# Optimization experiments

Hardware: AMD Instinct MI355X
Metric: run time of the kernel (lower is better)

The kernel has to match this reference:

```python
import jax, jax.numpy as jnp
import numpy as np

B, S, D = 8, 1024, 768
H, HD = 12, 64  # heads, head dim (H*HD == D)
EPS = 1e-12


def setup_inputs() -> dict:
    key = jax.random.key(0)
    ks = jax.random.split(key, 8)
    s = 0.02
    return {
        "hidden_states": jax.random.normal(ks[0], (B, S, D), jnp.float32),
        "attention_mask": jnp.zeros((B, 1, 1, S), jnp.float32),
        "head_mask": jnp.ones((H,), jnp.float32),
        "Wq": jax.random.normal(ks[1], (D, H * HD), jnp.float32) * s,
        "bq": jnp.zeros((H * HD,), jnp.float32),
        "Wk": jax.random.normal(ks[2], (D, H * HD), jnp.float32) * s,
        "bk": jnp.zeros((H * HD,), jnp.float32),
        "Wv": jax.random.normal(ks[3], (D, H * HD), jnp.float32) * s,
        "bv": jnp.zeros((H * HD,), jnp.float32),
        "Wo": jax.random.normal(ks[4], (D, H * HD), jnp.float32) * s,  # torch Linear weight [out=D, in=H*HD]
        "bo": jnp.zeros((D,), jnp.float32),
        "gamma": jnp.ones((D,), jnp.float32),
        "beta": jnp.zeros((D,), jnp.float32),
    }


def reference(hidden_states, attention_mask, head_mask, Wq, bq, Wk, bk, Wv, bv, Wo, bo, gamma, beta):
    def heads(x):  # [B,S,H*HD] -> [B,H,S,HD]
        return x.reshape(B, S, H, HD).transpose(0, 2, 1, 3)

    q = heads(hidden_states @ Wq.T + bq)
    k = heads(hidden_states @ Wk.T + bk)
    v = heads(hidden_states @ Wv.T + bv)

    scores = jnp.einsum("bhqd,bhkd->bhqk", q, k) / np.sqrt(HD).astype(np.float32)
    scores = scores + attention_mask
    probs = jax.nn.softmax(scores, axis=-1)  # dropout p=0 (eval)
    ctx = jnp.einsum("bhqk,bhkd->bhqd", probs, v)  # [B,H,S,HD]

    # masked per-head output projection: Wo.T.view(H, HD, D)
    Wph = Wo.T.reshape(H, HD, D)
    proj = jnp.einsum("bhsd,hde,h->bse", ctx, Wph, head_mask) + bo

    # residual + LayerNorm
    x = proj + hidden_states
    mu = jnp.mean(x, axis=-1, keepdims=True)
    var = jnp.mean(jnp.square(x - mu), axis=-1, keepdims=True)
    out = (x - mu) * jax.lax.rsqrt(var + EPS) * gamma + beta
    return out
```

## Files before the change

### kernel.cpp

```cpp
#include <hip/hip_runtime.h>
#include <hip/hip_bf16.h>
#include <math.h>

#define Bn 8
#define Sn 1024
#define Dn 768
#define Hn 12
#define MROWS (Bn * Sn)

typedef __attribute__((ext_vector_type(8))) short short8;
typedef __attribute__((ext_vector_type(4))) float floatx4;

__device__ __forceinline__ unsigned short f2b(float x) {
    union { float f; unsigned u; } v; v.f = x;
    unsigned r = v.u + 0x7fffu + ((v.u >> 16) & 1u);
    return (unsigned short)(r >> 16);
}

__device__ __forceinline__ void gload16(const void* g, void* l) {
    __builtin_amdgcn_global_load_lds(
        (const __attribute__((address_space(1))) void*)g,
        (__attribute__((address_space(3))) void*)l, 16, 0, 0);
}

__global__ __launch_bounds__(256) void convert_all(const float* __restrict__ X,
                                                   const float* __restrict__ Wq, const float* __restrict__ Wk,
                                                   const float* __restrict__ Wv, const float* __restrict__ Wo,
                                                   unsigned short* __restrict__ Xb,
                                                   unsigned short* __restrict__ Wqb, unsigned short* __restrict__ Wkb,
                                                   unsigned short* __restrict__ Wvb, unsigned short* __restrict__ Wob) {
    const int id = blockIdx.x;
    const float* src;
    unsigned short* dst;
    int i;
    if (id < 6144) {
        src = X; dst = Xb;
        i = id * 256 + threadIdx.x;
    } else {
        const int y = (id - 6144) / 576;
        src = (y == 0) ? Wq : (y == 1) ? Wk : (y == 2) ? Wv : Wo;
        dst = (y == 0) ? Wqb : (y == 1) ? Wkb : (y == 2) ? Wvb : Wob;
        i = ((id - 6144) % 576) * 256 + threadIdx.x;
    }
    float4 v = reinterpret_cast<const float4*>(src)[i];
    ushort4 o;
    o.x = f2b(v.x); o.y = f2b(v.y); o.z = f2b(v.z); o.w = f2b(v.w);
    reinterpret_cast<ushort4*>(dst)[i] = o;
}

__global__ __launch_bounds__(256) void gemm_qkv(const unsigned short* __restrict__ A,
                                                const unsigned short* __restrict__ Wq,
                                                const unsigned short* __restrict__ Wk,
                                                const unsigned short* __restrict__ Wv,
                                                const float* __restrict__ bq,
                                                const float* __restrict__ bk,
                                                const float* __restrict__ bv,
                                                unsigned short* __restrict__ Qh,
                                                unsigned short* __restrict__ Kh,
                                                unsigned short* __restrict__ Vt) {
    __shared__ __align__(16) unsigned short As[128 * 64];
    __shared__ __align__(16) unsigned short Ws[128 * 64];
    const int id = blockIdx.x;
    const int by = id & 63;
    const int bx = id >> 6;
    const int mat = bx / 6;
    const int m0 = by * 128;
    const int n0 = (bx % 6) * 128;
    const unsigned short* W = (mat == 0) ? Wq : (mat == 1) ? Wk : Wv;
    const float* bias = (mat == 0) ? bq : (mat == 1) ? bk : bv;
    unsigned short* Cout = (mat == 0) ? Qh : (mat == 1) ? Kh : Vt;

    const int tid = threadIdx.x;
    const int w = tid >> 6, l = tid & 63, quad = l >> 4, mr = l & 15;
    const int wm = (w >> 1) * 64, wn = (w & 1) * 64;

    const unsigned short* gAsrc[4];
    const unsigned short* gWsrc[4];
    unsigned short* lAdst[4];
    unsigned short* lWdst[4];
#pragma unroll
    for (int j = 0; j < 4; j++) {
        const int u = tid + j * 256;
        const int r = u >> 3, c = u & 7;
        const int kq = (c ^ (r & 7)) * 8;
        gAsrc[j] = &A[(size_t)(m0 + r) * Dn + kq];
        gWsrc[j] = &W[(size_t)(n0 + r) * Dn + kq];
        lAdst[j] = &As[u * 8];
        lWdst[j] = &Ws[u * 8];
    }

    int aoff[4][2], woff[4][2];
#pragma unroll
    for (int i = 0; i < 4; i++) {
        const int ra = wm + i * 16 + mr;
        const int rw = wn + i * 16 + mr;
#pragma unroll
        for (int ks = 0; ks < 2; ks++) {
            aoff[i][ks] = (ra * 8 + ((quad + ks * 4) ^ (ra & 7))) * 8;
            woff[i][ks] = (rw * 8 + ((quad + ks * 4) ^ (rw & 7))) * 8;
        }
    }

    floatx4 acc[4][4];
#pragma unroll
    for (int i = 0; i < 4; i++)
#pragma unroll
        for (int j = 0; j < 4; j++) {
            floatx4 z = {0.f, 0.f, 0.f, 0.f};
            acc[i][j] = z;
        }

    for (int kt = 0; kt < 12; kt++) {
        const int k0 = kt * 64;
        __syncthreads();
#pragma unroll
        for (int j = 0; j < 4; j++) {
            gload16(gAsrc[j] + k0, lAdst[j]);
            gload16(gWsrc[j] + k0, lWdst[j]);
        }
        __syncthreads();

        short8 af[4][2], bf[4][2];
#pragma unroll
        for (int i = 0; i < 4; i++)
#pragma unroll
            for (int ks = 0; ks < 2; ks++) {
                af[i][ks] = *(const short8*)&As[aoff[i][ks]];
                bf[i][ks] = *(const short8*)&Ws[woff[i][ks]];
            }
#pragma unroll
        for (int ks = 0; ks < 2; ks++)
#pragma unroll
            for (int i = 0; i < 4; i++)
#pragma unroll
                for (int j = 0; j < 4; j++)
                    acc[i][j] = __builtin_amdgcn_mfma_f32_16x16x32_bf16(af[i][ks], bf[j][ks], acc[i][j], 0, 0, 0);
    }

#pragma unroll
    for (int j = 0; j < 4; j++) {
        const int col = n0 + wn + j * 16 + mr;
        const float bval = bias[col];
        const int h = col >> 6, d = col & 63;
#pragma unroll
        for (int i = 0; i < 4; i++) {
#pragma unroll
            for (int r = 0; r < 4; r++) {
                const int m = m0 + wm + i * 16 + quad * 4 + r;
                const float val = acc[i][j][r] + bval;
                const int b = m >> 10, s = m & 1023;
                const size_t base = (size_t)(b * Hn + h) << 16;
                if (mat == 2)
                    Cout[base + (size_t)d * 1024 + s] = f2b(val);
                else
                    Cout[base + (size_t)s * 64 + d] = f2b(val);
            }
        }
    }
}

__global__ __launch_bounds__(256) void gemm_out(const unsigned short* __restrict__ A,
                                                const unsigned short* __restrict__ W,
                                                const float* __restrict__ bias,
                                                const float* __restrict__ X,
                                                float* __restrict__ xres) {
    __shared__ __align__(16) unsigned short As[64 * 64];
    __shared__ __align__(16) unsigned short Ws[128 * 64];
    const int id = blockIdx.x;
    const int by = id & 127;
    const int bx = id >> 7;
    const int m0 = by * 64;
    const int n0 = bx * 128;

    const int tid = threadIdx.x;
    const int w = tid >> 6, l = tid & 63, quad = l >> 4, mr = l & 15;

    const unsigned short* gAsrc[2];
    unsigned short* lAdst[2];
#pragma unroll
    for (int j = 0; j < 2; j++) {
        const int u = tid + j * 256;
        const int r = u >> 3, c = u & 7;
        gAsrc[j] = &A[(size_t)(m0 + r) * Dn + (c ^ (r & 7)) * 8];
        lAdst[j] = &As[u * 8];
    }
    const unsigned short* gWsrc[4];
    unsigned short* lWdst[4];
#pragma unroll
    for (int j = 0; j < 4; j++) {
        const int u = tid + j * 256;
        const int r = u >> 3, c = u & 7;
        gWsrc[j] = &W[(size_t)(n0 + r) * Dn + (c ^ (r & 7)) * 8];
        lWdst[j] = &Ws[u * 8];
    }

    int aoff[4][2], woff[2][2];
#pragma unroll
    for (int i = 0; i < 4; i++) {
        const int ra = i * 16 + mr;
#pragma unroll
        for (int ks = 0; ks < 2; ks++)
            aoff[i][ks] = (ra * 8 + ((quad + ks * 4) ^ (ra & 7))) * 8;
    }
#pragma unroll
    for (int j = 0; j < 2; j++) {
        const int rw = w * 32 + j * 16 + mr;
#pragma unroll
        for (int ks = 0; ks < 2; ks++)
            woff[j][ks] = (rw * 8 + ((quad + ks * 4) ^ (rw & 7))) * 8;
    }

    floatx4 acc[4][2];
#pragma unroll
    for (int i = 0; i < 4; i++)
#pragma unroll
        for (int j = 0; j < 2; j++) {
            floatx4 z = {0.f, 0.f, 0.f, 0.f};
            acc[i][j] = z;
        }

    for (int kt = 0; kt < 12; kt++) {
        const int k0 = kt * 64;
        __syncthreads();
#pragma unroll
        for (int j = 0; j < 2; j++) gload16(gAsrc[j] + k0, lAdst[j]);
#pragma unroll
        for (int j = 0; j < 4; j++) gload16(gWsrc[j] + k0, lWdst[j]);
        __syncthreads();

        short8 af[4][2], bf[2][2];
#pragma unroll
        for (int i = 0; i < 4; i++)
#pragma unroll
            for (int ks = 0; ks < 2; ks++)
                af[i][ks] = *(const short8*)&As[aoff[i][ks]];
#pragma unroll
        for (int j = 0; j < 2; j++)
#pragma unroll
            for (int ks = 0; ks < 2; ks++)
                bf[j][ks] = *(const short8*)&Ws[woff[j][ks]];
#pragma unroll
        for (int ks = 0; ks < 2; ks++)
#pragma unroll
            for (int i = 0; i < 4; i++)
#pragma unroll
                for (int j = 0; j < 2; j++)
                    acc[i][j] = __builtin_amdgcn_mfma_f32_16x16x32_bf16(af[i][ks], bf[j][ks], acc[i][j], 0, 0, 0);
    }

#pragma unroll
    for (int j = 0; j < 2; j++) {
        const int col = n0 + w * 32 + j * 16 + mr;
        const float bval = bias[col];
#pragma unroll
        for (int i = 0; i < 4; i++) {
#pragma unroll
            for (int r = 0; r < 4; r++) {
                const int m = m0 + i * 16 + quad * 4 + r;
                xres[(size_t)m * Dn + col] = acc[i][j][r] + bval + X[(size_t)m * Dn + col];
            }
        }
    }
}

__global__ __launch_bounds__(256) void flash_attn_mfma(const unsigned short* __restrict__ Qh,
                                                       const unsigned short* __restrict__ Kh,
                                                       const unsigned short* __restrict__ Vt,
                                                       const float* __restrict__ mask,
                                                       const float* __restrict__ head_mask,
                                                       unsigned short* __restrict__ ctx) {
    __shared__ __align__(16) unsigned short Ks[64 * 72];
    __shared__ __align__(16) unsigned short Vs[64 * 72];
    __shared__ __align__(16) unsigned short Ps[128 * 72];
    __shared__ float msk[64];

    const int id = blockIdx.x;
    const int bh = id % 96;
    const int qt = id / 96;
    const int b = bh / Hn, h = bh % Hn;
    const int q0 = qt * 128;
    const int tid = threadIdx.x;
    const int w = tid >> 6, l = tid & 63, quad = l >> 4, mr = l & 15;
    const size_t hb = (size_t)(b * Hn + h) << 16;

    short8 aq[2][2];
#pragma unroll
    for (int i = 0; i < 2; i++)
#pragma unroll
        for (int ks = 0; ks < 2; ks++)
            aq[i][ks] = *(const short8*)&Qh[hb + (size_t)(q0 + w * 32 + i * 16 + mr) * 64 + ks * 32 + quad * 8];

    float l_s[2][4];
    floatx4 oacc[2][4];
#pragma unroll
    for (int i = 0; i < 2; i++) {
#pragma unroll
        for (int r = 0; r < 4; r++) l_s[i][r] = 0.f;
#pragma unroll
        for (int jj = 0; jj < 4; jj++) {
            floatx4 z = {0.f, 0.f, 0.f, 0.f};
            oacc[i][jj] = z;
        }
    }

    const int srow = tid >> 2;
    const int scol = (tid & 3) * 16;

    short8 pk0 = *(const short8*)&Kh[hb + (size_t)srow * 64 + scol];
    short8 pk1 = *(const short8*)&Kh[hb + (size_t)srow * 64 + scol + 8];
    short8 pv0 = *(const short8*)&Vt[hb + (size_t)srow * 1024 + scol];
    short8 pv1 = *(const short8*)&Vt[hb + (size_t)srow * 1024 + scol + 8];
    float pm = mask[b * Sn + (tid & 63)];

    for (int kt = 0; kt < Sn / 64; kt++) {
        __syncthreads();
        *(short8*)&Ks[srow * 72 + scol] = pk0;
        *(short8*)&Ks[srow * 72 + scol + 8] = pk1;
        *(short8*)&Vs[srow * 72 + scol] = pv0;
        *(short8*)&Vs[srow * 72 + scol + 8] = pv1;
        if (tid < 64) msk[tid] = pm;
        if (kt < Sn / 64 - 1) {
            const int k0 = (kt + 1) * 64;
            pk0 = *(const short8*)&Kh[hb + (size_t)(k0 + srow) * 64 + scol];
            pk1 = *(const short8*)&Kh[hb + (size_t)(k0 + srow) * 64 + scol + 8];
            pv0 = *(const short8*)&Vt[hb + (size_t)srow * 1024 + k0 + scol];
            pv1 = *(const short8*)&Vt[hb + (size_t)srow * 1024 + k0 + scol + 8];
            pm = mask[b * Sn + k0 + (tid & 63)];
        }
        __syncthreads();

        floatx4 sacc[2][4];
#pragma unroll
        for (int i = 0; i < 2; i++)
#pragma unroll
            for (int j = 0; j < 4; j++) {
                floatx4 z = {0.f, 0.f, 0.f, 0.f};
                sacc[i][j] = z;
            }
#pragma unroll
        for (int ks = 0; ks < 2; ks++) {
#pragma unroll
            for (int j = 0; j < 4; j++) {
                short8 bk = *(const short8*)&Ks[(j * 16 + mr) * 72 + ks * 32 + quad * 8];
                sacc[0][j] = __builtin_amdgcn_mfma_f32_16x16x32_bf16(aq[0][ks], bk, sacc[0][j], 0, 0, 0);
                sacc[1][j] = __builtin_amdgcn_mfma_f32_16x16x32_bf16(aq[1][ks], bk, sacc[1][j], 0, 0, 0);
            }
        }

#pragma unroll
        for (int i = 0; i < 2; i++) {
#pragma unroll
            for (int j = 0; j < 4; j++) {
                const float mk = msk[j * 16 + mr];
#pragma unroll
                for (int r = 0; r < 4; r++) {
                    const float p = __expf(sacc[i][j][r] * 0.125f + mk);
                    l_s[i][r] += p;
                    Ps[(w * 32 + i * 16 + quad * 4 + r) * 72 + j * 16 + mr] = f2b(p);
                }
            }
        }

#pragma unroll
        for (int ks = 0; ks < 2; ks++) {
            short8 ap0 = *(const short8*)&Ps[(w * 32 + mr) * 72 + ks * 32 + quad * 8];
            short8 ap1 = *(const short8*)&Ps[(w * 32 + 16 + mr) * 72 + ks * 32 + quad * 8];
#pragma unroll
            for (int jj = 0; jj < 4; jj++) {
                short8 bv = *(const short8*)&Vs[(jj * 16 + mr) * 72 + ks * 32 + quad * 8];
                oacc[0][jj] = __builtin_amdgcn_mfma_f32_16x16x32_bf16(ap0, bv, oacc[0][jj], 0, 0, 0);
                oacc[1][jj] = __builtin_amdgcn_mfma_f32_16x16x32_bf16(ap1, bv, oacc[1][jj], 0, 0, 0);
            }
        }
    }

    const float hm = head_mask[h];
    float inv[2][4];
#pragma unroll
    for (int i = 0; i < 2; i++)
#pragma unroll
        for (int r = 0; r < 4; r++) {
            float t = l_s[i][r];
            t += __shfl_xor(t, 1);
            t += __shfl_xor(t, 2);
            t += __shfl_xor(t, 4);
            t += __shfl_xor(t, 8);
            inv[i][r] = hm / t;
        }
#pragma unroll
    for (int i = 0; i < 2; i++)
#pragma unroll
        for (int jj = 0; jj < 4; jj++)
#pragma unroll
            for (int r = 0; r < 4; r++) {
                const int qrow = q0 + w * 32 + i * 16 + quad * 4 + r;
                ctx[(size_t)(b * Sn + qrow) * Dn + h * 64 + jj * 16 + mr] = f2b(oacc[i][jj][r] * inv[i][r]);
            }
}

__global__ __launch_bounds__(256) void ln_kernel(const float* __restrict__ x,
                                                 const float* __restrict__ gamma,
                                                 const float* __restrict__ beta,
                                                 float* __restrict__ out) {
    __shared__ float r1[4];
    __shared__ float r2[4];
    const int m = blockIdx.x;
    const int tid = threadIdx.x;
    const int w = tid >> 6, lane = tid & 63;

    float xv[3];
    float s = 0.f, ss = 0.f;
#pragma unroll
    for (int i = 0; i < 3; i++) {
        int j = tid + i * 256;
        float t = x[(size_t)m * Dn + j];
        xv[i] = t;
        s += t;
        ss += t * t;
    }
#pragma unroll
    for (int o = 1; o < 64; o <<= 1) {
        s += __shfl_xor(s, o);
        ss += __shfl_xor(ss, o);
    }
    if (lane == 0) { r1[w] = s; r2[w] = ss; }
    __syncthreads();
    const float sum = r1[0] + r1[1] + r1[2] + r1[3];
    const float sqs = r2[0] + r2[1] + r2[2] + r2[3];
    const float mu = sum * (1.0f / Dn);
    const float var = sqs * (1.0f / Dn) - mu * mu;
    const float rstd = rsqrtf(var + 1e-12f);
#pragma unroll
    for (int i = 0; i < 3; i++) {
        int j = tid + i * 256;
        out[(size_t)m * Dn + j] = (xv[i] - mu) * rstd * gamma[j] + beta[j];
    }
}

extern "C" void kernel_launch(void* const* d_in, const int* in_sizes, int n_in,
                              void* d_out, int out_size, void* d_ws, size_t ws_size,
                              hipStream_t stream) {
    const float* X         = (const float*)d_in[0];
    const float* mask      = (const float*)d_in[1];
    const float* head_mask = (const float*)d_in[2];
    const float* Wq        = (const float*)d_in[3];
    const float* bq        = (const float*)d_in[4];
    const float* Wk        = (const float*)d_in[5];
    const float* bk        = (const float*)d_in[6];
    const float* Wv        = (const float*)d_in[7];
    const float* bv        = (const float*)d_in[8];
    const float* Wo        = (const float*)d_in[9];
    const float* bo        = (const float*)d_in[10];
    const float* gamma     = (const float*)d_in[11];
    const float* beta      = (const float*)d_in[12];
    float* out = (float*)d_out;

    const size_t NE = (size_t)Bn * Sn * Dn;
    const size_t NW = (size_t)Dn * Dn;

    char* p = (char*)d_ws;
    unsigned short* Xb  = (unsigned short*)p;  p += NE * 2;
    unsigned short* Wqb = (unsigned short*)p;  p += NW * 2;
    unsigned short* Wkb = (unsigned short*)p;  p += NW * 2;
    unsigned short* Wvb = (unsigned short*)p;  p += NW * 2;
    unsigned short* Wob = (unsigned short*)p;  p += NW * 2;
    unsigned short* Qh  = (unsigned short*)p;  p += NE * 2;
    unsigned short* Kh  = (unsigned short*)p;  p += NE * 2;
    unsigned short* Vtb = (unsigned short*)p;  p += NE * 2;
    unsigned short* ctx = (unsigned short*)p;  p += NE * 2;
    float* xres = (float*)p;

    convert_all<<<8448, 256, 0, stream>>>(X, Wq, Wk, Wv, Wo, Xb, Wqb, Wkb, Wvb, Wob);

    gemm_qkv<<<1152, 256, 0, stream>>>(Xb, Wqb, Wkb, Wvb, bq, bk, bv, Qh, Kh, Vtb);

    flash_attn_mfma<<<768, 256, 0, stream>>>(Qh, Kh, Vtb, mask, head_mask, ctx);

    gemm_out<<<768, 256, 0, stream>>>(ctx, Wob, bo, X, xres);

    ln_kernel<<<MROWS, 256, 0, stream>>>(xres, gamma, beta, out);
}
```

Baseline: 233.1 us.

## Fuse fp32-to-bf16 conversion into GEMM loads and transpose attention MFMA layout

Removes the separate conversion kernel and its bf16 workspace copies. Both GEMMs now read fp32 directly, convert in registers and store to LDS, with register-prefetch of the next tile replacing the async global-to-LDS loads. The attention kernel swaps MFMA operand roles so scores come out transposed: the mask is staged once per block in shared memory, probabilities are written as packed pairs, and ctx is stored with vectorized packed writes. This trades one kernel launch and an extra pass over X for twice the global read traffic in the QKV GEMM and more register pressure.

```diff
diff --git a/kernel.cpp b/kernel.cpp
--- a/kernel.cpp
+++ b/kernel.cpp
@@ -17,41 +17,23 @@
     return (unsigned short)(r >> 16);
 }
 
-__device__ __forceinline__ void gload16(const void* g, void* l) {
-    __builtin_amdgcn_global_load_lds(
-        (const __attribute__((address_space(1))) void*)g,
-        (__attribute__((address_space(3))) void*)l, 16, 0, 0);
-}
-
-__global__ __launch_bounds__(256) void convert_all(const float* __restrict__ X,
-                                                   const float* __restrict__ Wq, const float* __restrict__ Wk,
-                                                   const float* __restrict__ Wv, const float* __restrict__ Wo,
-                                                   unsigned short* __restrict__ Xb,
-                                                   unsigned short* __restrict__ Wqb, unsigned short* __restrict__ Wkb,
-                                                   unsigned short* __restrict__ Wvb, unsigned short* __restrict__ Wob) {
-    const int id = blockIdx.x;
-    const float* src;
-    unsigned short* dst;
-    int i;
-    if (id < 6144) {
-        src = X; dst = Xb;
-        i = id * 256 + threadIdx.x;
-    } else {
-        const int y = (id - 6144) / 576;
-        src = (y == 0) ? Wq : (y == 1) ? Wk : (y == 2) ? Wv : Wo;
-        dst = (y == 0) ? Wqb : (y == 1) ? Wkb : (y == 2) ? Wvb : Wob;
-        i = ((id - 6144) % 576) * 256 + threadIdx.x;
-    }
-    float4 v = reinterpret_cast<const float4*>(src)[i];
-    ushort4 o;
-    o.x = f2b(v.x); o.y = f2b(v.y); o.z = f2b(v.z); o.w = f2b(v.w);
-    reinterpret_cast<ushort4*>(dst)[i] = o;
-}
-
-__global__ __launch_bounds__(256) void gemm_qkv(const unsigned short* __restrict__ A,
-                                                const unsigned short* __restrict__ Wq,
-                                                const unsigned short* __restrict__ Wk,
-                                                const unsigned short* __restrict__ Wv,
+__device__ __forceinline__ unsigned pk2(float a, float b) {
+    union { __hip_bfloat162 h2; unsigned u; } cv;
+    cv.h2 = __float22bfloat162_rn(float2{a, b});
+    return cv.u;
+}
+
+__device__ __forceinline__ uint4 pk8(float4 a, float4 b) {
+    uint4 r;
+    r.x = pk2(a.x, a.y); r.y = pk2(a.z, a.w);
+    r.z = pk2(b.x, b.y); r.w = pk2(b.z, b.w);
+    return r;
+}
+
+__global__ __launch_bounds__(256) void gemm_qkv(const float* __restrict__ Xf,
+                                                const float* __restrict__ Wqf,
+                                                const float* __restrict__ Wkf,
+                                                const float* __restrict__ Wvf,
                                                 const float* __restrict__ bq,
                                                 const float* __restrict__ bk,
                                                 const float* __restrict__ bv,
@@ -66,7 +48,7 @@
     const int mat = bx / 6;
     const int m0 = by * 128;
     const int n0 = (bx % 6) * 128;
-    const unsigned short* W = (mat == 0) ? Wq : (mat == 1) ? Wk : Wv;
+    const float* W = (mat == 0) ? Wqf : (mat == 1) ? Wkf : Wvf;
     const float* bias = (mat == 0) ? bq : (mat == 1) ? bk : bv;
     unsigned short* Cout = (mat == 0) ? Qh : (mat == 1) ? Kh : Vt;
 
@@ -74,19 +56,19 @@
     const int w = tid >> 6, l = tid & 63, quad = l >> 4, mr = l & 15;
     const int wm = (w >> 1) * 64, wn = (w & 1) * 64;
 
-    const unsigned short* gAsrc[4];
-    const unsigned short* gWsrc[4];
-    unsigned short* lAdst[4];
-    unsigned short* lWdst[4];
+    const float* gA[4];
+    const float* gW[4];
+    unsigned short* lA[4];
+    unsigned short* lW[4];
 #pragma unroll
     for (int j = 0; j < 4; j++) {
         const int u = tid + j * 256;
         const int r = u >> 3, c = u & 7;
         const int kq = (c ^ (r & 7)) * 8;
-        gAsrc[j] = &A[(size_t)(m0 + r) * Dn + kq];
-        gWsrc[j] = &W[(size_t)(n0 + r) * Dn + kq];
-        lAdst[j] = &As[u * 8];
-        lWdst[j] = &Ws[u * 8];
+        gA[j] = &Xf[(size_t)(m0 + r) * Dn + kq];
+        gW[j] = &W[(size_t)(n0 + r) * Dn + kq];
+        lA[j] = &As[u * 8];
+        lW[j] = &Ws[u * 8];
     }
 
     int aoff[4][2], woff[4][2];
@@ -110,31 +92,54 @@
             acc[i][j] = z;
         }
 
+    float4 fa[4][2], fw[4][2];
+#pragma unroll
+    for (int j = 0; j < 4; j++) {
+        fa[j][0] = *(const float4*)(gA[j]);
+        fa[j][1] = *(const float4*)(gA[j] + 4);
+        fw[j][0] = *(const float4*)(gW[j]);
+        fw[j][1] = *(const float4*)(gW[j] + 4);
+    }
+
     for (int kt = 0; kt < 12; kt++) {
-        const int k0 = kt * 64;
-        __syncthreads();
+        uint4 ca[4], cw[4];
 #pragma unroll
         for (int j = 0; j < 4; j++) {
-            gload16(gAsrc[j] + k0, lAdst[j]);
-            gload16(gWsrc[j] + k0, lWdst[j]);
-        }
-        __syncthreads();
-
-        short8 af[4][2], bf[4][2];
-#pragma unroll
-        for (int i = 0; i < 4; i++)
-#pragma unroll
-            for (int ks = 0; ks < 2; ks++) {
-                af[i][ks] = *(const short8*)&As[aoff[i][ks]];
-                bf[i][ks] = *(const short8*)&Ws[woff[i][ks]];
-            }
-#pragma unroll
-        for (int ks = 0; ks < 2; ks++)
+            ca[j] = pk8(fa[j][0], fa[j][1]);
+            cw[j] = pk8(fw[j][0], fw[j][1]);
+        }
+        __syncthreads();
+#pragma unroll
+        for (int j = 0; j < 4; j++) {
+            *(uint4*)lA[j] = ca[j];
+            *(uint4*)lW[j] = cw[j];
+        }
+        __syncthreads();
+        if (kt < 11) {
+            const int k0 = (kt + 1) * 64;
+#pragma unroll
+            for (int j = 0; j < 4; j++) {
+                fa[j][0] = *(const float4*)(gA[j] + k0);
+                fa[j][1] = *(const float4*)(gA[j] + k0 + 4);
+                fw[j][0] = *(const float4*)(gW[j] + k0);
+                fw[j][1] = *(const float4*)(gW[j] + k0 + 4);
+            }
+        }
+
+#pragma unroll
+        for (int ks = 0; ks < 2; ks++) {
+            short8 af[4], bf[4];
+#pragma unroll
+            for (int i = 0; i < 4; i++) {
+                af[i] = *(const short8*)&As[aoff[i][ks]];
+                bf[i] = *(const short8*)&Ws[woff[i][ks]];
+            }
 #pragma unroll
             for (int i = 0; i < 4; i++)
 #pragma unroll
                 for (int j = 0; j < 4; j++)
-                    acc[i][j] = __builtin_amdgcn_mfma_f32_16x16x32_bf16(af[i][ks], bf[j][ks], acc[i][j], 0, 0, 0);
+                    acc[i][j] = __builtin_amdgcn_mfma_f32_16x16x32_bf16(af[i], bf[j], acc[i][j], 0, 0, 0);
+        }
     }
 
 #pragma unroll
@@ -160,7 +165,7 @@
 }
 
 __global__ __launch_bounds__(256) void gemm_out(const unsigned short* __restrict__ A,
-                                                const unsigned short* __restrict__ W,
+                                                const float* __restrict__ Wf,
                                                 const float* __restrict__ bias,
                                                 const float* __restrict__ X,
                                                 float* __restrict__ xres) {
@@ -175,23 +180,23 @@
     const int tid = threadIdx.x;
     const int w = tid >> 6, l = tid & 63, quad = l >> 4, mr = l & 15;
 
-    const unsigned short* gAsrc[2];
-    unsigned short* lAdst[2];
+    const unsigned short* gA[2];
+    unsigned short* lA[2];
 #pragma unroll
     for (int j = 0; j < 2; j++) {
         const int u = tid + j * 256;
         const int r = u >> 3, c = u & 7;
-        gAsrc[j] = &A[(size_t)(m0 + r) * Dn + (c ^ (r & 7)) * 8];
-        lAdst[j] = &As[u * 8];
-    }
-    const unsigned short* gWsrc[4];
-    unsigned short* lWdst[4];
+        gA[j] = &A[(size_t)(m0 + r) * Dn + (c ^ (r & 7)) * 8];
+        lA[j] = &As[u * 8];
+    }
+    const float* gW[4];
+    unsigned short* lW[4];
 #pragma unroll
     for (int j = 0; j < 4; j++) {
         const int u = tid + j * 256;
         const int r = u >> 3, c = u & 7;
-        gWsrc[j] = &W[(size_t)(n0 + r) * Dn + (c ^ (r & 7)) * 8];
-        lWdst[j] = &Ws[u * 8];
+        gW[j] = &Wf[(size_t)(n0 + r) * Dn + (c ^ (r & 7)) * 8];
+        lW[j] = &Ws[u * 8];
     }
 
     int aoff[4][2], woff[2][2];
@@ -219,33 +224,50 @@
             acc[i][j] = z;
         }
 
+    uint4 ua[2];
+    float4 fw[4][2];
+#pragma unroll
+    for (int j = 0; j < 2; j++) ua[j] = *(const uint4*)(gA[j]);
+#pragma unroll
+    for (int j = 0; j < 4; j++) {
+        fw[j][0] = *(const float4*)(gW[j]);
+        fw[j][1] = *(const float4*)(gW[j] + 4);
+    }
+
     for (int kt = 0; kt < 12; kt++) {
-        const int k0 = kt * 64;
-        __syncthreads();
-#pragma unroll
-        for (int j = 0; j < 2; j++) gload16(gAsrc[j] + k0, lAdst[j]);
-#pragma unroll
-        for (int j = 0; j < 4; j++) gload16(gWsrc[j] + k0, lWdst[j]);
-        __syncthreads();
-
-        short8 af[4][2], bf[2][2];
-#pragma unroll
-        for (int i = 0; i < 4; i++)
-#pragma unroll
-            for (int ks = 0; ks < 2; ks++)
-                af[i][ks] = *(const short8*)&As[aoff[i][ks]];
-#pragma unroll
-        for (int j = 0; j < 2; j++)
-#pragma unroll
-            for (int ks = 0; ks < 2; ks++)
-                bf[j][ks] = *(const short8*)&Ws[woff[j][ks]];
-#pragma unroll
-        for (int ks = 0; ks < 2; ks++)
+        uint4 cw[4];
+#pragma unroll
+        for (int j = 0; j < 4; j++) cw[j] = pk8(fw[j][0], fw[j][1]);
+        __syncthreads();
+#pragma unroll
+        for (int j = 0; j < 2; j++) *(uint4*)lA[j] = ua[j];
+#pragma unroll
+        for (int j = 0; j < 4; j++) *(uint4*)lW[j] = cw[j];
+        __syncthreads();
+        if (kt < 11) {
+            const int k0 = (kt + 1) * 64;
+#pragma unroll
+            for (int j = 0; j < 2; j++) ua[j] = *(const uint4*)(gA[j] + k0 / 1 + 0 * k0), ua[j] = *(const uint4*)(gA[j] + k0);
+#pragma unroll
+            for (int j = 0; j < 4; j++) {
+                fw[j][0] = *(const float4*)(gW[j] + k0);
+                fw[j][1] = *(const float4*)(gW[j] + k0 + 4);
+            }
+        }
+
+#pragma unroll
+        for (int ks = 0; ks < 2; ks++) {
+            short8 af[4], bf[2];
+#pragma unroll
+            for (int i = 0; i < 4; i++) af[i] = *(const short8*)&As[aoff[i][ks]];
+#pragma unroll
+            for (int j = 0; j < 2; j++) bf[j] = *(const short8*)&Ws[woff[j][ks]];
 #pragma unroll
             for (int i = 0; i < 4; i++)
 #pragma unroll
                 for (int j = 0; j < 2; j++)
-                    acc[i][j] = __builtin_amdgcn_mfma_f32_16x16x32_bf16(af[i][ks], bf[j][ks], acc[i][j], 0, 0, 0);
+                    acc[i][j] = __builtin_amdgcn_mfma_f32_16x16x32_bf16(af[i], bf[j], acc[i][j], 0, 0, 0);
+        }
     }
 
 #pragma unroll
@@ -272,7 +294,7 @@
     __shared__ __align__(16) unsigned short Ks[64 * 72];
     __shared__ __align__(16) unsigned short Vs[64 * 72];
     __shared__ __align__(16) unsigned short Ps[128 * 72];
-    __shared__ float msk[64];
+    __shared__ __align__(16) float mskAll[1024];
 
     const int id = blockIdx.x;
     const int bh = id % 96;
@@ -283,25 +305,24 @@
     const int w = tid >> 6, l = tid & 63, quad = l >> 4, mr = l & 15;
     const size_t hb = (size_t)(b * Hn + h) << 16;
 
-    short8 aq[2][2];
-#pragma unroll
-    for (int i = 0; i < 2; i++)
+    *(float4*)&mskAll[tid * 4] = *(const float4*)&mask[b * Sn + tid * 4];
+
+    short8 bq[2][2];
+#pragma unroll
+    for (int n = 0; n < 2; n++)
 #pragma unroll
         for (int ks = 0; ks < 2; ks++)
-            aq[i][ks] = *(const short8*)&Qh[hb + (size_t)(q0 + w * 32 + i * 16 + mr) * 64 + ks * 32 + quad * 8];
-
-    float l_s[2][4];
-    floatx4 oacc[2][4];
-#pragma unroll
-    for (int i = 0; i < 2; i++) {
-#pragma unroll
-        for (int r = 0; r < 4; r++) l_s[i][r] = 0.f;
-#pragma unroll
-        for (int jj = 0; jj < 4; jj++) {
+            bq[n][ks] = *(const short8*)&Qh[hb + (size_t)(q0 + w * 32 + n * 16 + mr) * 64 + ks * 32 + quad * 8];
+
+    float l_acc[2] = {0.f, 0.f};
+    floatx4 oacc[4][2];
+#pragma unroll
+    for (int dt = 0; dt < 4; dt++)
+#pragma unroll
+        for (int n = 0; n < 2; n++) {
             floatx4 z = {0.f, 0.f, 0.f, 0.f};
-            oacc[i][jj] = z;
-        }
-    }
+            oacc[dt][n] = z;
+        }
 
     const int srow = tid >> 2;
     const int scol = (tid & 3) * 16;
@@ -310,7 +331,6 @@
     short8 pk1 = *(const short8*)&Kh[hb + (size_t)srow * 64 + scol + 8];
     short8 pv0 = *(const short8*)&Vt[hb + (size_t)srow * 1024 + scol];
     short8 pv1 = *(const short8*)&Vt[hb + (size_t)srow * 1024 + scol + 8];
-    float pm = mask[b * Sn + (tid & 63)];
 
     for (int kt = 0; kt < Sn / 64; kt++) {
         __syncthreads();
@@ -318,84 +338,84 @@
         *(short8*)&Ks[srow * 72 + scol + 8] = pk1;
         *(short8*)&Vs[srow * 72 + scol] = pv0;
         *(short8*)&Vs[srow * 72 + scol + 8] = pv1;
-        if (tid < 64) msk[tid] = pm;
         if (kt < Sn / 64 - 1) {
             const int k0 = (kt + 1) * 64;
             pk0 = *(const short8*)&Kh[hb + (size_t)(k0 + srow) * 64 + scol];
             pk1 = *(const short8*)&Kh[hb + (size_t)(k0 + srow) * 64 + scol + 8];
             pv0 = *(const short8*)&Vt[hb + (size_t)srow * 1024 + k0 + scol];
             pv1 = *(const short8*)&Vt[hb + (size_t)srow * 1024 + k0 + scol + 8];
-            pm = mask[b * Sn + k0 + (tid & 63)];
-        }
-        __syncthreads();
-
-        floatx4 sacc[2][4];
-#pragma unroll
-        for (int i = 0; i < 2; i++)
-#pragma unroll
-            for (int j = 0; j < 4; j++) {
+        }
+        __syncthreads();
+
+        floatx4 sacc[4][2];
+#pragma unroll
+        for (int i = 0; i < 4; i++)
+#pragma unroll
+            for (int n = 0; n < 2; n++) {
                 floatx4 z = {0.f, 0.f, 0.f, 0.f};
-                sacc[i][j] = z;
+                sacc[i][n] = z;
             }
 #pragma unroll
         for (int ks = 0; ks < 2; ks++) {
 #pragma unroll
-            for (int j = 0; j < 4; j++) {
-                short8 bk = *(const short8*)&Ks[(j * 16 + mr) * 72 + ks * 32 + quad * 8];
-                sacc[0][j] = __builtin_amdgcn_mfma_f32_16x16x32_bf16(aq[0][ks], bk, sacc[0][j], 0, 0, 0);
-                sacc[1][j] = __builtin_amdgcn_mfma_f32_16x16x32_bf16(aq[1][ks], bk, sacc[1][j], 0, 0, 0);
-            }
-        }
-
-#pragma unroll
-        for (int i = 0; i < 2; i++) {
-#pragma unroll
-            for (int j = 0; j < 4; j++) {
-                const float mk = msk[j * 16 + mr];
-#pragma unroll
-                for (int r = 0; r < 4; r++) {
-                    const float p = __expf(sacc[i][j][r] * 0.125f + mk);
-                    l_s[i][r] += p;
-                    Ps[(w * 32 + i * 16 + quad * 4 + r) * 72 + j * 16 + mr] = f2b(p);
-                }
+            for (int i = 0; i < 4; i++) {
+                short8 ak = *(const short8*)&Ks[(i * 16 + mr) * 72 + ks * 32 + quad * 8];
+                sacc[i][0] = __builtin_amdgcn_mfma_f32_16x16x32_bf16(ak, bq[0][ks], sacc[i][0], 0, 0, 0);
+                sacc[i][1] = __builtin_amdgcn_mfma_f32_16x16x32_bf16(ak, bq[1][ks], sacc[i][1], 0, 0, 0);
+            }
+        }
+
+#pragma unroll
+        for (int i = 0; i < 4; i++) {
+            const float4 cm = *(const float4*)&mskAll[kt * 64 + i * 16 + quad * 4];
+#pragma unroll
+            for (int n = 0; n < 2; n++) {
+                const float p0 = __expf(sacc[i][n][0] * 0.125f + cm.x);
+                const float p1 = __expf(sacc[i][n][1] * 0.125f + cm.y);
+                const float p2 = __expf(sacc[i][n][2] * 0.125f + cm.z);
+                const float p3 = __expf(sacc[i][n][3] * 0.125f + cm.w);
+                l_acc[n] += p0 + p1 + p2 + p3;
+                uint2 pp;
+                pp.x = pk2(p0, p1);
+                pp.y = pk2(p2, p3);
+                *(uint2*)&Ps[(w * 32 + n * 16 + mr) * 72 + i * 16 + quad * 4] = pp;
             }
         }
 
 #pragma unroll
         for (int ks = 0; ks < 2; ks++) {
-            short8 ap0 = *(const short8*)&Ps[(w * 32 + mr) * 72 + ks * 32 + quad * 8];
-            short8 ap1 = *(const short8*)&Ps[(w * 32 + 16 + mr) * 72 + ks * 32 + quad * 8];
-#pragma unroll
-            for (int jj = 0; jj < 4; jj++) {
-                short8 bv = *(const short8*)&Vs[(jj * 16 + mr) * 72 + ks * 32 + quad * 8];
-                oacc[0][jj] = __builtin_amdgcn_mfma_f32_16x16x32_bf16(ap0, bv, oacc[0][jj], 0, 0, 0);
-                oacc[1][jj] = __builtin_amdgcn_mfma_f32_16x16x32_bf16(ap1, bv, oacc[1][jj], 0, 0, 0);
+            short8 bp0 = *(const short8*)&Ps[(w * 32 + mr) * 72 + ks * 32 + quad * 8];
+            short8 bp1 = *(const short8*)&Ps[(w * 32 + 16 + mr) * 72 + ks * 32 + quad * 8];
+#pragma unroll
+            for (int dt = 0; dt < 4; dt++) {
+                short8 av = *(const short8*)&Vs[(dt * 16 + mr) * 72 + ks * 32 + quad * 8];
+                oacc[dt][0] = __builtin_amdgcn_mfma_f32_16x16x32_bf16(av, bp0, oacc[dt][0], 0, 0, 0);
+                oacc[dt][1] = __builtin_amdgcn_mfma_f32_16x16x32_bf16(av, bp1, oacc[dt][1], 0, 0, 0);
             }
         }
     }
 
     const float hm = head_mask[h];
-    float inv[2][4];
-#pragma unroll
-    for (int i = 0; i < 2; i++)
-#pragma unroll
-        for (int r = 0; r < 4; r++) {
-            float t = l_s[i][r];
-            t += __shfl_xor(t, 1);
-            t += __shfl_xor(t, 2);
-            t += __shfl_xor(t, 4);
-            t += __shfl_xor(t, 8);
-            inv[i][r] = hm / t;
-        }
-#pragma unroll
-    for (int i = 0; i < 2; i++)
-#pragma unroll
-        for (int jj = 0; jj < 4; jj++)
-#pragma unroll
-            for (int r = 0; r < 4; r++) {
-                const int qrow = q0 + w * 32 + i * 16 + quad * 4 + r;
-                ctx[(size_t)(b * Sn + qrow) * Dn + h * 64 + jj * 16 + mr] = f2b(oacc[i][jj][r] * inv[i][r]);
-            }
+    float inv[2];
+#pragma unroll
+    for (int n = 0; n < 2; n++) {
+        float t = l_acc[n];
+        t += __shfl_xor(t, 16);
+        t += __shfl_xor(t, 32);
+        inv[n] = hm / t;
+    }
+#pragma unroll
+    for (int n = 0; n < 2; n++) {
+        const int q = q0 + w * 32 + n * 16 + mr;
+        unsigned short* dst = &ctx[(size_t)(b * Sn + q) * Dn + h * 64 + quad * 4];
+#pragma unroll
+        for (int dt = 0; dt < 4; dt++) {
+            uint2 pp;
+            pp.x = pk2(oacc[dt][n][0] * inv[n], oacc[dt][n][1] * inv[n]);
+            pp.y = pk2(oacc[dt][n][2] * inv[n], oacc[dt][n][3] * inv[n]);
+            *(uint2*)&dst[dt * 16] = pp;
+        }
+    }
 }
 
 __global__ __launch_bounds__(256) void ln_kernel(const float* __restrict__ x,
@@ -456,27 +476,19 @@
     float* out = (float*)d_out;
 
     const size_t NE = (size_t)Bn * Sn * Dn;
-    const size_t NW = (size_t)Dn * Dn;
 
     char* p = (char*)d_ws;
-    unsigned short* Xb  = (unsigned short*)p;  p += NE * 2;
-    unsigned short* Wqb = (unsigned short*)p;  p += NW * 2;
-    unsigned short* Wkb = (unsigned short*)p;  p += NW * 2;
-    unsigned short* Wvb = (unsigned short*)p;  p += NW * 2;
-    unsigned short* Wob = (unsigned short*)p;  p += NW * 2;
     unsigned short* Qh  = (unsigned short*)p;  p += NE * 2;
     unsigned short* Kh  = (unsigned short*)p;  p += NE * 2;
     unsigned short* Vtb = (unsigned short*)p;  p += NE * 2;
     unsigned short* ctx = (unsigned short*)p;  p += NE * 2;
     float* xres = (float*)p;
 
-    convert_all<<<8448, 256, 0, stream>>>(X, Wq, Wk, Wv, Wo, Xb, Wqb, Wkb, Wvb, Wob);
-
-    gemm_qkv<<<1152, 256, 0, stream>>>(Xb, Wqb, Wkb, Wvb, bq, bk, bv, Qh, Kh, Vtb);
+    gemm_qkv<<<1152, 256, 0, stream>>>(X, Wq, Wk, Wv, bq, bk, bv, Qh, Kh, Vtb);
 
     flash_attn_mfma<<<768, 256, 0, stream>>>(Qh, Kh, Vtb, mask, head_mask, ctx);
 
-    gemm_out<<<768, 256, 0, stream>>>(ctx, Wob, bo, X, xres);
+    gemm_out<<<768, 256, 0, stream>>>(ctx, Wo, bo, X, xres);
 
     ln_kernel<<<MROWS, 256, 0, stream>>>(xres, gamma, beta, out);
 }
```

Measured after the change: 259.5 us. 11.3% more time.
